# Kernel tuning notes

Measured on AMD Instinct MI355X. Metric: run time of the kernel, lower is better.

The kernel has to match this reference:

```python
import jax, jax.numpy as jnp
import numpy as np
import math

L, D, H, DK, DFF, B, S = 4, 512, 8, 256, 2048, 8, 256
HD = H * DK
EPS = 1e-6


def _norm(x, alpha, bias):
    # torch: alpha*(x-mean)/(std_unbiased + eps) + bias  (std uses ddof=1)
    mu = x.mean(axis=-1, keepdims=True)
    var = ((x - mu) ** 2).sum(axis=-1, keepdims=True) / (x.shape[-1] - 1)
    return alpha * (x - mu) / (jnp.sqrt(var) + EPS) + bias


def _positional_encoding():
    pos = jnp.arange(S, dtype=jnp.float32)[:, None]          # [S,1]
    i = jnp.arange(0, D, 2, dtype=jnp.float32)               # even indices
    pe_sin = jnp.sin(pos / (S ** (2.0 * i / D)))             # [S,D/2]
    pe_cos = jnp.cos(pos / (S ** (2.0 * (i + 1.0) / D)))     # [S,D/2]
    pe = jnp.zeros((S, D), dtype=jnp.float32)
    pe = pe.at[:, 0::2].set(pe_sin).at[:, 1::2].set(pe_cos)
    return pe


def setup_inputs() -> dict:
    key = jax.random.key(0)
    ks = jax.random.split(key, 16)
    sc = 0.02
    inp = {
        "data": jax.random.normal(ks[0], (B, S, D), dtype=jnp.float32),
        "attn_m": jax.random.randint(ks[1], (B, S), 0, 2, dtype=jnp.int32),
        "view_idx": 0,
        "seg_emb": jax.random.normal(ks[2], (3, D), dtype=jnp.float32) * sc,
        "Wq": jax.random.normal(ks[3], (L, D, HD), dtype=jnp.float32) * sc,
        "bq": jnp.zeros((L, HD), dtype=jnp.float32),
        "Wk": jax.random.normal(ks[4], (L, D, HD), dtype=jnp.float32) * sc,
        "bk": jnp.zeros((L, HD), dtype=jnp.float32),
        "Wv": jax.random.normal(ks[5], (L, D, HD), dtype=jnp.float32) * sc,
        "bv": jnp.zeros((L, HD), dtype=jnp.float32),
        "Wo": jax.random.normal(ks[6], (L, HD, D), dtype=jnp.float32) * sc,
        "bo": jnp.zeros((L, D), dtype=jnp.float32),
        "W1": jax.random.normal(ks[7], (L, D, DFF), dtype=jnp.float32) * sc,
        "b1": jnp.zeros((L, DFF), dtype=jnp.float32),
        "W2": jax.random.normal(ks[8], (L, DFF, D), dtype=jnp.float32) * sc,
        "b2": jnp.zeros((L, D), dtype=jnp.float32),
        "alpha1": jnp.ones((L, D), dtype=jnp.float32),
        "bias1": jnp.zeros((L, D), dtype=jnp.float32),
        "alpha2": jnp.ones((L, D), dtype=jnp.float32),
        "bias2": jnp.zeros((L, D), dtype=jnp.float32),
        "alpha_f": jnp.ones((D,), dtype=jnp.float32),
        "bias_f": jnp.zeros((D,), dtype=jnp.float32),
    }
    return inp


def reference(data, attn_m, view_idx, seg_emb, Wq, bq, Wk, bk, Wv, bv, Wo, bo,
              W1, b1, W2, b2, alpha1, bias1, alpha2, bias2, alpha_f, bias_f):
    # positional encoder: x*sqrt(d_f) + pe + seg_embedding(view_idx*seq_len)
    pe = _positional_encoding()
    seg_idx = view_idx * S  # scalar; must be < 3 (view_idx == 0 in practice)
    x = data * math.sqrt(D) + pe[None, :, :] + seg_emb[seg_idx][None, None, :]

    # mask: attn_m [B,S] -> [B,1,1,S] bool, True = masked (key axis)
    maskb = attn_m.astype(bool)[:, None, None, :]

    for i in range(L):
        x2 = _norm(x, alpha1[i], bias1[i])
        q = (x2 @ Wq[i] + bq[i]).reshape(B, S, H, DK).transpose(0, 2, 1, 3)
        k = (x2 @ Wk[i] + bk[i]).reshape(B, S, H, DK).transpose(0, 2, 1, 3)
        v = (x2 @ Wv[i] + bv[i]).reshape(B, S, H, DK).transpose(0, 2, 1, 3)
        scores = jnp.einsum('bhqd,bhkd->bhqk', q, k) / math.sqrt(DK)
        scores = jnp.where(maskb, -1e9, scores)
        attnw = jax.nn.softmax(scores, axis=-1)
        o = jnp.einsum('bhqk,bhkd->bhqd', attnw, v)
        o = o.transpose(0, 2, 1, 3).reshape(B, S, HD) @ Wo[i] + bo[i]
        x = x + o
        x2 = _norm(x, alpha2[i], bias2[i])
        ff = jax.nn.relu(x2 @ W1[i] + b1[i]) @ W2[i] + b2[i]
        x = x + ff

    return _norm(x, alpha_f, bias_f)
```

## Files before the change

### kernel.cpp

```cpp
#include <hip/hip_runtime.h>
#include <hip/hip_bf16.h>

#define LNUM 4
#define DIM  512
#define SS   256

typedef unsigned short ushort_t;
typedef __attribute__((ext_vector_type(8))) short bf16x8;
typedef __attribute__((ext_vector_type(4))) float f32x4;

#define VWAIT(n) asm volatile("s_waitcnt vmcnt(" #n ")" ::: "memory")
__device__ __forceinline__ void bar() { __builtin_amdgcn_s_barrier(); }

__device__ __forceinline__ ushort_t f2b(float f) {
  union { float f; unsigned u; } x; x.f = f;
  unsigned r = x.u + 0x7FFFu + ((x.u >> 16) & 1u);
  return (ushort_t)(r >> 16);
}

__device__ __forceinline__ void gload16(const void* g, void* s) {
  __builtin_amdgcn_global_load_lds((const __attribute__((address_space(1))) void*)g,
                                   (__attribute__((address_space(3))) void*)s, 16, 0, 0);
}

template<int TM, int TN, int EPI>
__global__ __launch_bounds__(256, 2)
void gemm_bt(const ushort_t* __restrict__ A, const ushort_t* __restrict__ B,
             const float* __restrict__ bias, const float* __restrict__ bias2,
             const float* __restrict__ bias3,
             ushort_t* __restrict__ outB, ushort_t* __restrict__ outB2,
             ushort_t* __restrict__ outB3, float* __restrict__ outF,
             int K, int lda, int ldb, int ldc, int nkz, int relu)
{
  constexpr int CA = TM / 32, CB = TN / 32, SN = CA + CB;
  constexpr int WM = TM / 32, WN = TN / 32;
  __shared__ ushort_t As[3 * TM * 64];
  __shared__ ushort_t Bs[3 * TN * 64];
  const int tid = threadIdx.x, lane = tid & 63, wid = tid >> 6;
  const int wm = wid >> 1, wn = wid & 1;
  const int kz = blockIdx.z, Kz = K / nkz, k0 = kz * Kz, nt = Kz >> 6;

  const ushort_t* Ab = A + (long)blockIdx.y * TM * lda + k0;
  const ushort_t* Bb = B + (long)blockIdx.x * TN * ldb + k0;

  const ushort_t* srcA[CA]; ushort_t* ldsA[CA];
  const ushort_t* srcB[CB]; ushort_t* ldsB[CB];
#pragma unroll
  for (int c = 0; c < CA; ++c) {
    int off = c * 4096 + tid * 16;
    int row = off >> 7;
    int scol = ((off & 127) ^ ((row & 7) << 4)) >> 1;
    srcA[c] = Ab + (long)row * lda + scol;
    ldsA[c] = As + c * 2048 + wid * 512;
  }
#pragma unroll
  for (int c = 0; c < CB; ++c) {
    int off = c * 4096 + tid * 16;
    int row = off >> 7;
    int scol = ((off & 127) ^ ((row & 7) << 4)) >> 1;
    srcB[c] = Bb + (long)row * ldb + scol;
    ldsB[c] = Bs + c * 2048 + wid * 512;
  }

  f32x4 acc[WM][WN] = {};

  auto STAGE = [&](int buf, int t) {
#pragma unroll
    for (int c = 0; c < CA; ++c) gload16(srcA[c] + t * 64, ldsA[c] + buf * TM * 64);
#pragma unroll
    for (int c = 0; c < CB; ++c) gload16(srcB[c] + t * 64, ldsB[c] + buf * TN * 64);
  };

  STAGE(0, 0);
  STAGE(1, 1);
  for (int t = 0; t < nt; ++t) {
    if (t < nt - 1) { if constexpr (SN == 6) VWAIT(6); else VWAIT(4); }
    else VWAIT(0);
    bar();
    if (t + 2 < nt) STAGE((t + 2) % 3, t + 2);
    const int buf = t % 3;
#pragma unroll
    for (int ks = 0; ks < 2; ++ks) {
      const int kb = ks * 64 + ((lane >> 4) << 4);
      bf16x8 af[WM], bfr[WN];
#pragma unroll
      for (int f = 0; f < WM; ++f) {
        int ra = wm * (TM / 2) + f * 16 + (lane & 15);
        af[f] = *(const bf16x8*)((const char*)As + buf * TM * 128 + ra * 128 + (kb ^ ((ra & 7) << 4)));
      }
#pragma unroll
      for (int g = 0; g < WN; ++g) {
        int rb = wn * (TN / 2) + g * 16 + (lane & 15);
        bfr[g] = *(const bf16x8*)((const char*)Bs + buf * TN * 128 + rb * 128 + (kb ^ ((rb & 7) << 4)));
      }
#pragma unroll
      for (int i = 0; i < WM; ++i)
#pragma unroll
        for (int j = 0; j < WN; ++j)
          acc[i][j] = __builtin_amdgcn_mfma_f32_16x16x32_bf16(af[i], bfr[j], acc[i][j], 0, 0, 0);
    }
  }

  const int row0 = blockIdx.y * TM + wm * (TM / 2) + ((lane >> 4) << 2);
  int col0 = blockIdx.x * TN + wn * (TN / 2) + (lane & 15);
  const float* bsel = bias;
  ushort_t* osel = outB;
  int seg = 0;
  if (EPI == 3) {
    seg = (blockIdx.x * TN) >> 11;
    if (seg == 1) { bsel = bias2; osel = outB2; }
    else if (seg == 2) { bsel = bias3; }
    col0 -= seg * 2048;
  }
#pragma unroll
  for (int i = 0; i < WM; ++i) {
#pragma unroll
    for (int j = 0; j < WN; ++j) {
      const int col = col0 + j * 16;
      float bv;
      if (EPI == 2) bv = (kz == 0) ? bias[col] : 0.f;
      else          bv = bsel[col];
#pragma unroll
      for (int r = 0; r < 4; ++r) {
        const int row = row0 + i * 16 + r;
        float v = acc[i][j][r] + bv;
        if (EPI == 2) {
          outF[(long)kz * 1048576 + (long)row * ldc + col] = v;
        } else if (EPI == 3 && seg == 2) {
          int bh = ((row >> 8) << 3) + (col >> 8);
          outB3[((long)bh << 16) + (long)(col & 255) * 256 + (row & 255)] = f2b(v);
        } else {
          if (relu) v = fmaxf(v, 0.f);
          osel[(long)row * ldc + col] = f2b(v);
        }
      }
    }
  }
}

__global__ __launch_bounds__(256)
void attn_k(const ushort_t* __restrict__ qb, const ushort_t* __restrict__ kbf,
            const ushort_t* __restrict__ vT, const int* __restrict__ attnm,
            ushort_t* __restrict__ ao)
{
  __shared__ ushort_t Qs[64 * 256];
  __shared__ ushort_t KV[3][64 * 256];
  __shared__ int smask[256];
  const int qt = blockIdx.x, bh = blockIdx.y, b = bh >> 3, h = bh & 7;
  const int tid = threadIdx.x, lane = tid & 63, wid = tid >> 6;

  smask[tid] = attnm[b * 256 + tid];
  VWAIT(0);

  int srow[8], scol[8];
#pragma unroll
  for (int c = 0; c < 8; ++c) {
    int off = c * 4096 + tid * 16;
    srow[c] = off >> 9;
    scol[c] = ((off & 511) ^ ((srow[c] & 7) << 4)) >> 1;
  }

#define STQ() do { _Pragma("unroll") for (int c = 0; c < 8; ++c) \
  gload16(qb + (long)(b * 256 + qt * 64 + srow[c]) * 2048 + h * 256 + scol[c], Qs + c * 2048 + wid * 512); } while (0)
#define STK(KC, DST) do { _Pragma("unroll") for (int c = 0; c < 8; ++c) \
  gload16(kbf + (long)(b * 256 + (KC) * 64 + srow[c]) * 2048 + h * 256 + scol[c], (DST) + c * 2048 + wid * 512); } while (0)
#define STV(VC, DST) do { _Pragma("unroll") for (int c = 0; c < 8; ++c) \
  gload16(vT + ((long)bh << 16) + (long)((VC) * 64 + srow[c]) * 256 + scol[c], (DST) + c * 2048 + wid * 512); } while (0)

  f32x4 accs[16] = {};
  f32x4 acco[4][4] = {};

#define QKC(IDX, KVB) do { _Pragma("unroll") \
  for (int ks = 0; ks < 8; ++ks) { \
    const int kb = ks * 64 + ((lane >> 4) << 4); \
    const int ra = wid * 16 + (lane & 15); \
    bf16x8 aq = *(const bf16x8*)((const char*)Qs + ra * 512 + (kb ^ ((ra & 7) << 4))); \
    _Pragma("unroll") \
    for (int j = 0; j < 4; ++j) { \
      const int rb = j * 16 + (lane & 15); \
      bf16x8 bk_ = *(const bf16x8*)((const char*)(KVB) + rb * 512 + (kb ^ ((rb & 7) << 4))); \
      accs[(IDX) * 4 + j] = __builtin_amdgcn_mfma_f32_16x16x32_bf16(aq, bk_, accs[(IDX) * 4 + j], 0, 0, 0); \
    } \
  } } while (0)

#define PVC(VC, KVB) do { _Pragma("unroll") \
  for (int ks = 0; ks < 8; ++ks) { \
    const int kb = ks * 64 + ((lane >> 4) << 4); \
    const int ra = wid * 16 + (lane & 15); \
    bf16x8 pa = *(const bf16x8*)((const char*)Qs + ra * 512 + (kb ^ ((ra & 7) << 4))); \
    _Pragma("unroll") \
    for (int j = 0; j < 4; ++j) { \
      const int rb = j * 16 + (lane & 15); \
      bf16x8 bv_ = *(const bf16x8*)((const char*)(KVB) + rb * 512 + (kb ^ ((rb & 7) << 4))); \
      acco[VC][j] = __builtin_amdgcn_mfma_f32_16x16x32_bf16(pa, bv_, acco[VC][j], 0, 0, 0); \
    } \
  } } while (0)

  STQ(); STK(0, KV[0]); STK(1, KV[1]);

  VWAIT(16); bar(); STK(2, KV[2]); QKC(0, KV[0]);
  VWAIT(8);  bar(); STK(3, KV[0]); QKC(1, KV[1]);
  VWAIT(8);  bar(); STV(0, KV[1]); QKC(2, KV[2]);
  VWAIT(8);  bar(); STV(1, KV[2]); QKC(3, KV[0]);

  bar();
  STV(2, KV[0]);

  {
    float mr[4] = {-3e38f, -3e38f, -3e38f, -3e38f}, sr[4] = {};
#pragma unroll
    for (int jj = 0; jj < 16; ++jj) {
      int key = jj * 16 + (lane & 15);
      bool mk = smask[key] != 0;
#pragma unroll
      for (int r = 0; r < 4; ++r) {
        float s = mk ? -1e9f : accs[jj][r] * 0.0625f;
        accs[jj][r] = s;
        mr[r] = fmaxf(mr[r], s);
      }
    }
#pragma unroll
    for (int o = 1; o < 16; o <<= 1)
#pragma unroll
      for (int r = 0; r < 4; ++r) mr[r] = fmaxf(mr[r], __shfl_xor(mr[r], o, 64));
#pragma unroll
    for (int jj = 0; jj < 16; ++jj)
#pragma unroll
      for (int r = 0; r < 4; ++r) {
        float e = __expf(accs[jj][r] - mr[r]);
        accs[jj][r] = e;
        sr[r] += e;
      }
#pragma unroll
    for (int o = 1; o < 16; o <<= 1)
#pragma unroll
      for (int r = 0; r < 4; ++r) sr[r] += __shfl_xor(sr[r], o, 64);
#pragma unroll
    for (int r = 0; r < 4; ++r) sr[r] = 1.f / sr[r];
#pragma unroll
    for (int jj = 0; jj < 16; ++jj)
#pragma unroll
      for (int r = 0; r < 4; ++r) {
        int prow = wid * 16 + ((lane >> 4) << 2) + r;
        int cb = (jj * 16 + (lane & 15)) * 2;
        *(ushort_t*)((char*)Qs + prow * 512 + (cb ^ ((prow & 7) << 4))) = f2b(accs[jj][r] * sr[r]);
      }
  }

  VWAIT(16); bar();                 PVC(0, KV[1]);
  VWAIT(8);  bar(); STV(3, KV[1]); PVC(1, KV[2]);
  VWAIT(8);  bar();                 PVC(2, KV[0]);
  VWAIT(0);  bar();                 PVC(3, KV[1]);

#pragma unroll
  for (int vc = 0; vc < 4; ++vc)
#pragma unroll
    for (int j = 0; j < 4; ++j)
#pragma unroll
      for (int r = 0; r < 4; ++r) {
        int q = qt * 64 + wid * 16 + ((lane >> 4) << 2) + r;
        int dk = vc * 64 + j * 16 + (lane & 15);
        ao[(long)(b * 256 + q) * 2048 + h * 256 + dk] = f2b(acco[vc][j][r]);
      }
#undef STQ
#undef STK
#undef STV
#undef QKC
#undef PVC
}

__global__ __launch_bounds__(256)
void build_x(const float* __restrict__ data, const float* __restrict__ seg,
             const int* __restrict__ viewp, float* __restrict__ x)
{
  int i = blockIdx.x * 256 + threadIdx.x;
  int d = i & 511;
  int s = (i >> 9) & 255;
  float ang = (float)s * exp2f((float)d * -0.03125f);
  float pe = (d & 1) ? cosf(ang) : sinf(ang);
  int vrow = viewp[0] * SS;
  x[i] = data[i] * 22.627416997969522f + pe + seg[vrow * DIM + d];
}

__global__ __launch_bounds__(256)
void lnorm_k(const float* __restrict__ x, const float* __restrict__ p0,
             const float* __restrict__ p1, float* __restrict__ xout,
             const float* __restrict__ alpha, const float* __restrict__ beta,
             ushort_t* __restrict__ outB, float* __restrict__ outF)
{
  const int row = blockIdx.x, tid = threadIdx.x;
  const long base = (long)row * DIM;
  float2 v = ((const float2*)(x + base))[tid];
  if (p0) {
    float2 a = ((const float2*)(p0 + base))[tid];
    float2 c = ((const float2*)(p1 + base))[tid];
    v.x += a.x + c.x; v.y += a.y + c.y;
    ((float2*)(xout + base))[tid] = v;
  }
  float s = v.x + v.y;
#pragma unroll
  for (int o = 32; o; o >>= 1) s += __shfl_xor(s, o, 64);
  __shared__ float rs[4], rq[4];
  if ((tid & 63) == 0) rs[tid >> 6] = s;
  __syncthreads();
  const float mu = (rs[0] + rs[1] + rs[2] + rs[3]) * (1.f / 512.f);
  const float dx = v.x - mu, dy = v.y - mu;
  float q = dx * dx + dy * dy;
#pragma unroll
  for (int o = 32; o; o >>= 1) q += __shfl_xor(q, o, 64);
  if ((tid & 63) == 0) rq[tid >> 6] = q;
  __syncthreads();
  const float var = (rq[0] + rq[1] + rq[2] + rq[3]) * (1.f / 511.f);
  const float rstd = 1.f / (sqrtf(var) + 1e-6f);
  const int d0 = tid * 2;
  const float o0 = alpha[d0] * dx * rstd + beta[d0];
  const float o1 = alpha[d0 + 1] * dy * rstd + beta[d0 + 1];
  if (outB) { outB[base + d0] = f2b(o0); outB[base + d0 + 1] = f2b(o1); }
  else      { outF[base + d0] = o0;      outF[base + d0 + 1] = o1; }
}

__global__ __launch_bounds__(256)
void wtrans(const float* __restrict__ in, ushort_t* __restrict__ out,
            int R, int C, long ozs)
{
  __shared__ float t[32][33];
  const int z = blockIdx.z;
  const long zi = (long)z * R * C, zo = (long)z * ozs;
  const int c0 = blockIdx.x * 32, r0 = blockIdx.y * 32;
  const int tx = threadIdx.x & 31, ty = threadIdx.x >> 5;
#pragma unroll
  for (int i = 0; i < 4; ++i) t[ty + i * 8][tx] = in[zi + (long)(r0 + ty + i * 8) * C + c0 + tx];
  __syncthreads();
#pragma unroll
  for (int i = 0; i < 4; ++i) out[zo + (long)(c0 + ty + i * 8) * R + r0 + tx] = f2b(t[tx][ty + i * 8]);
}

extern "C" void kernel_launch(void* const* d_in, const int* in_sizes, int n_in,
                              void* d_out, int out_size, void* d_ws, size_t ws_size,
                              hipStream_t stream)
{
  const float* data  = (const float*)d_in[0];
  const int*   attnm = (const int*)d_in[1];
  const int*   viewp = (const int*)d_in[2];
  const float* seg   = (const float*)d_in[3];
  const float* Wq    = (const float*)d_in[4];
  const float* bq    = (const float*)d_in[5];
  const float* Wk    = (const float*)d_in[6];
  const float* bk    = (const float*)d_in[7];
  const float* Wv    = (const float*)d_in[8];
  const float* bv    = (const float*)d_in[9];
  const float* Wo    = (const float*)d_in[10];
  const float* bo    = (const float*)d_in[11];
  const float* W1    = (const float*)d_in[12];
  const float* b1    = (const float*)d_in[13];
  const float* W2    = (const float*)d_in[14];
  const float* b2    = (const float*)d_in[15];
  const float* al1   = (const float*)d_in[16];
  const float* be1   = (const float*)d_in[17];
  const float* al2   = (const float*)d_in[18];
  const float* be2   = (const float*)d_in[19];
  const float* alf   = (const float*)d_in[20];
  const float* bef   = (const float*)d_in[21];

  char* w = (char*)d_ws;
  const size_t MB = 1024 * 1024;
  ushort_t* qkvW = (ushort_t*)(w + 0 * MB);
  ushort_t* WoT  = (ushort_t*)(w + 24 * MB);
  ushort_t* W1T  = (ushort_t*)(w + 32 * MB);
  ushort_t* W2T  = (ushort_t*)(w + 40 * MB);
  float*    x    = (float*)   (w + 48 * MB);
  ushort_t* x2   = (ushort_t*)(w + 52 * MB);
  ushort_t* qb   = (ushort_t*)(w + 54 * MB);
  ushort_t* kbf  = (ushort_t*)(w + 62 * MB);
  ushort_t* vT   = (ushort_t*)(w + 70 * MB);
  ushort_t* ao   = (ushort_t*)(w + 78 * MB);
  ushort_t* ffh  = (ushort_t*)(w + 86 * MB);
  float*    pA   = (float*)   (w + 94 * MB);
  float*    pB   = (float*)   (w + 98 * MB);

  dim3 blk(256);
  const long QKV_L = 6144L * 512;
  wtrans<<<dim3(64, 16, 4), blk, 0, stream>>>(Wq, qkvW + 0 * 2048 * 512, 512, 2048, QKV_L);
  wtrans<<<dim3(64, 16, 4), blk, 0, stream>>>(Wk, qkvW + 1 * 2048 * 512, 512, 2048, QKV_L);
  wtrans<<<dim3(64, 16, 4), blk, 0, stream>>>(Wv, qkvW + 2 * 2048 * 512, 512, 2048, QKV_L);
  wtrans<<<dim3(16, 64, 4), blk, 0, stream>>>(Wo, WoT, 2048, 512, 512L * 2048);
  wtrans<<<dim3(64, 16, 4), blk, 0, stream>>>(W1, W1T, 512, 2048, 2048L * 512);
  wtrans<<<dim3(16, 64, 4), blk, 0, stream>>>(W2, W2T, 2048, 512, 512L * 2048);
  build_x<<<4096, blk, 0, stream>>>(data, seg, viewp, x);

  for (int i = 0; i < LNUM; ++i) {
    if (i == 0)
      lnorm_k<<<2048, blk, 0, stream>>>(x, nullptr, nullptr, nullptr,
                                        al1, be1, x2, nullptr);
    gemm_bt<128, 64, 3><<<dim3(96, 16, 1), blk, 0, stream>>>(
        x2, qkvW + (long)i * QKV_L, bq + i * 2048, bk + i * 2048, bv + i * 2048,
        qb, kbf, vT, nullptr, 512, 512, 512, 2048, 1, 0);
    attn_k<<<dim3(4, 64), blk, 0, stream>>>(qb, kbf, vT, attnm, ao);
    gemm_bt<64, 64, 2><<<dim3(8, 32, 2), blk, 0, stream>>>(
        ao, WoT + (long)i * 512 * 2048, bo + i * 512, nullptr, nullptr,
        nullptr, nullptr, nullptr, pA, 2048, 2048, 2048, 512, 2, 0);
    lnorm_k<<<2048, blk, 0, stream>>>(x, pA, pB, x, al2 + i * 512, be2 + i * 512, x2, nullptr);
    gemm_bt<128, 64, 0><<<dim3(32, 16, 1), blk, 0, stream>>>(
        x2, W1T + (long)i * 2048 * 512, b1 + i * 2048, nullptr, nullptr,
        ffh, nullptr, nullptr, nullptr, 512, 512, 512, 2048, 1, 1);
    gemm_bt<64, 64, 2><<<dim3(8, 32, 2), blk, 0, stream>>>(
        ffh, W2T + (long)i * 512 * 2048, b2 + i * 512, nullptr, nullptr,
        nullptr, nullptr, nullptr, pA, 2048, 2048, 2048, 512, 2, 0);
    if (i < LNUM - 1)
      lnorm_k<<<2048, blk, 0, stream>>>(x, pA, pB, x, al1 + (i + 1) * 512, be1 + (i + 1) * 512, x2, nullptr);
    else
      lnorm_k<<<2048, blk, 0, stream>>>(x, pA, pB, x, alf, bef, nullptr, (float*)d_out);
  }
}
```

Before: 474.6 us.

## Stage V transpose through LDS, raise MFMA priority, split-K four ways

The QKV GEMM epilogue for the V segment now writes the biased bf16 tile transposed into shared memory and then stores contiguous 16-byte chunks to the transposed V buffer. This replaces scattered 2-byte strided global writes. s_setprio is raised around the MFMA blocks in both the GEMM and attention kernels so matrix work gets issue priority over other waves. The Wo and W2 GEMMs move from split-K 2 to 4 to launch more blocks, and layernorm sums a variable number of fp32 partials, which costs extra partial-buffer traffic.

```diff
diff --git a/kernel.cpp b/kernel.cpp
--- a/kernel.cpp
+++ b/kernel.cpp
@@ -8,6 +8,7 @@
 typedef unsigned short ushort_t;
 typedef __attribute__((ext_vector_type(8))) short bf16x8;
 typedef __attribute__((ext_vector_type(4))) float f32x4;
+typedef __attribute__((ext_vector_type(8))) unsigned short u16x8;
 
 #define VWAIT(n) asm volatile("s_waitcnt vmcnt(" #n ")" ::: "memory")
 __device__ __forceinline__ void bar() { __builtin_amdgcn_s_barrier(); }
@@ -93,11 +94,13 @@
         int rb = wn * (TN / 2) + g * 16 + (lane & 15);
         bfr[g] = *(const bf16x8*)((const char*)Bs + buf * TN * 128 + rb * 128 + (kb ^ ((rb & 7) << 4)));
       }
+      __builtin_amdgcn_s_setprio(1);
 #pragma unroll
       for (int i = 0; i < WM; ++i)
 #pragma unroll
         for (int j = 0; j < WN; ++j)
           acc[i][j] = __builtin_amdgcn_mfma_f32_16x16x32_bf16(af[i], bfr[j], acc[i][j], 0, 0, 0);
+      __builtin_amdgcn_s_setprio(0);
     }
   }
 
@@ -112,6 +115,36 @@
     else if (seg == 2) { bsel = bias3; }
     col0 -= seg * 2048;
   }
+
+  if (EPI == 3 && seg == 2) {
+    ushort_t* Vt = As;
+    bar();
+#pragma unroll
+    for (int i = 0; i < WM; ++i)
+#pragma unroll
+      for (int j = 0; j < WN; ++j) {
+        const int colL = wn * (TN / 2) + j * 16 + (lane & 15);
+        const float bv = bsel[(col0 + j * 16) & 2047];
+#pragma unroll
+        for (int r = 0; r < 4; ++r) {
+          const int rowL = wm * (TM / 2) + i * 16 + ((lane >> 4) << 2) + r;
+          Vt[colL * 136 + rowL] = f2b(acc[i][j][r] + bv);
+        }
+      }
+    bar();
+    const int colvBase = blockIdx.x * TN - 4096;
+    const int h = colvBase >> 8, dk0 = colvBase & 255;
+    const int rowBase = blockIdx.y * TM;
+    const int bh = ((rowBase >> 8) << 3) + h;
+    const int s0 = rowBase & 255;
+    const int dkl = tid >> 2, scc = (tid & 3) * 32;
+    ushort_t* dst = outB3 + ((long)bh << 16) + (long)(dk0 + dkl) * 256 + s0 + scc;
+#pragma unroll
+    for (int m = 0; m < 4; ++m)
+      *(u16x8*)(dst + m * 8) = *(const u16x8*)(Vt + dkl * 136 + scc + m * 8);
+    return;
+  }
+
 #pragma unroll
   for (int i = 0; i < WM; ++i) {
 #pragma unroll
@@ -126,9 +159,6 @@
         float v = acc[i][j][r] + bv;
         if (EPI == 2) {
           outF[(long)kz * 1048576 + (long)row * ldc + col] = v;
-        } else if (EPI == 3 && seg == 2) {
-          int bh = ((row >> 8) << 3) + (col >> 8);
-          outB3[((long)bh << 16) + (long)(col & 255) * 256 + (row & 255)] = f2b(v);
         } else {
           if (relu) v = fmaxf(v, 0.f);
           osel[(long)row * ldc + col] = f2b(v);
@@ -170,7 +200,7 @@
   f32x4 accs[16] = {};
   f32x4 acco[4][4] = {};
 
-#define QKC(IDX, KVB) do { _Pragma("unroll") \
+#define QKC(IDX, KVB) do { __builtin_amdgcn_s_setprio(1); _Pragma("unroll") \
   for (int ks = 0; ks < 8; ++ks) { \
     const int kb = ks * 64 + ((lane >> 4) << 4); \
     const int ra = wid * 16 + (lane & 15); \
@@ -181,9 +211,9 @@
       bf16x8 bk_ = *(const bf16x8*)((const char*)(KVB) + rb * 512 + (kb ^ ((rb & 7) << 4))); \
       accs[(IDX) * 4 + j] = __builtin_amdgcn_mfma_f32_16x16x32_bf16(aq, bk_, accs[(IDX) * 4 + j], 0, 0, 0); \
     } \
-  } } while (0)
-
-#define PVC(VC, KVB) do { _Pragma("unroll") \
+  } __builtin_amdgcn_s_setprio(0); } while (0)
+
+#define PVC(VC, KVB) do { __builtin_amdgcn_s_setprio(1); _Pragma("unroll") \
   for (int ks = 0; ks < 8; ++ks) { \
     const int kb = ks * 64 + ((lane >> 4) << 4); \
     const int ra = wid * 16 + (lane & 15); \
@@ -194,7 +224,7 @@
       bf16x8 bv_ = *(const bf16x8*)((const char*)(KVB) + rb * 512 + (kb ^ ((rb & 7) << 4))); \
       acco[VC][j] = __builtin_amdgcn_mfma_f32_16x16x32_bf16(pa, bv_, acco[VC][j], 0, 0, 0); \
     } \
-  } } while (0)
+  } __builtin_amdgcn_s_setprio(0); } while (0)
 
   STQ(); STK(0, KV[0]); STK(1, KV[1]);
 
@@ -283,18 +313,19 @@
 }
 
 __global__ __launch_bounds__(256)
-void lnorm_k(const float* __restrict__ x, const float* __restrict__ p0,
-             const float* __restrict__ p1, float* __restrict__ xout,
+void lnorm_k(const float* __restrict__ x, const float* __restrict__ parts, int np,
+             float* __restrict__ xout,
              const float* __restrict__ alpha, const float* __restrict__ beta,
              ushort_t* __restrict__ outB, float* __restrict__ outF)
 {
   const int row = blockIdx.x, tid = threadIdx.x;
   const long base = (long)row * DIM;
   float2 v = ((const float2*)(x + base))[tid];
-  if (p0) {
-    float2 a = ((const float2*)(p0 + base))[tid];
-    float2 c = ((const float2*)(p1 + base))[tid];
-    v.x += a.x + c.x; v.y += a.y + c.y;
+  if (np) {
+    for (int p = 0; p < np; ++p) {
+      float2 a = ((const float2*)(parts + (long)p * 1048576 + base))[tid];
+      v.x += a.x; v.y += a.y;
+    }
     ((float2*)(xout + base))[tid] = v;
   }
   float s = v.x + v.y;
@@ -375,8 +406,7 @@
   ushort_t* vT   = (ushort_t*)(w + 70 * MB);
   ushort_t* ao   = (ushort_t*)(w + 78 * MB);
   ushort_t* ffh  = (ushort_t*)(w + 86 * MB);
-  float*    pA   = (float*)   (w + 94 * MB);
-  float*    pB   = (float*)   (w + 98 * MB);
+  float*    parts= (float*)   (w + 94 * MB);
 
   dim3 blk(256);
   const long QKV_L = 6144L * 512;
@@ -390,25 +420,24 @@
 
   for (int i = 0; i < LNUM; ++i) {
     if (i == 0)
-      lnorm_k<<<2048, blk, 0, stream>>>(x, nullptr, nullptr, nullptr,
-                                        al1, be1, x2, nullptr);
+      lnorm_k<<<2048, blk, 0, stream>>>(x, nullptr, 0, nullptr, al1, be1, x2, nullptr);
     gemm_bt<128, 64, 3><<<dim3(96, 16, 1), blk, 0, stream>>>(
         x2, qkvW + (long)i * QKV_L, bq + i * 2048, bk + i * 2048, bv + i * 2048,
         qb, kbf, vT, nullptr, 512, 512, 512, 2048, 1, 0);
     attn_k<<<dim3(4, 64), blk, 0, stream>>>(qb, kbf, vT, attnm, ao);
-    gemm_bt<64, 64, 2><<<dim3(8, 32, 2), blk, 0, stream>>>(
+    gemm_bt<64, 64, 2><<<dim3(8, 32, 4), blk, 0, stream>>>(
         ao, WoT + (long)i * 512 * 2048, bo + i * 512, nullptr, nullptr,
-        nullptr, nullptr, nullptr, pA, 2048, 2048, 2048, 512, 2, 0);
-    lnorm_k<<<2048, blk, 0, stream>>>(x, pA, pB, x, al2 + i * 512, be2 + i * 512, x2, nullptr);
+        nullptr, nullptr, nullptr, parts, 2048, 2048, 2048, 512, 4, 0);
+    lnorm_k<<<2048, blk, 0, stream>>>(x, parts, 4, x, al2 + i * 512, be2 + i * 512, x2, nullptr);
     gemm_bt<128, 64, 0><<<dim3(32, 16, 1), blk, 0, stream>>>(
         x2, W1T + (long)i * 2048 * 512, b1 + i * 2048, nullptr, nullptr,
         ffh, nullptr, nullptr, nullptr, 512, 512, 512, 2048, 1, 1);
-    gemm_bt<64, 64, 2><<<dim3(8, 32, 2), blk, 0, stream>>>(
+    gemm_bt<64, 64, 2><<<dim3(8, 32, 4), blk, 0, stream>>>(
         ffh, W2T + (long)i * 512 * 2048, b2 + i * 512, nullptr, nullptr,
-        nullptr, nullptr, nullptr, pA, 2048, 2048, 2048, 512, 2, 0);
+        nullptr, nullptr, nullptr, parts, 2048, 2048, 2048, 512, 4, 0);
     if (i < LNUM - 1)
-      lnorm_k<<<2048, blk, 0, stream>>>(x, pA, pB, x, al1 + (i + 1) * 512, be1 + (i + 1) * 512, x2, nullptr);
+      lnorm_k<<<2048, blk, 0, stream>>>(x, parts, 4, x, al1 + (i + 1) * 512, be1 + (i + 1) * 512, x2, nullptr);
     else
-      lnorm_k<<<2048, blk, 0, stream>>>(x, pA, pB, x, alf, bef, nullptr, (float*)d_out);
-  }
-}
+      lnorm_k<<<2048, blk, 0, stream>>>(x, parts, 4, x, alf, bef, nullptr, (float*)d_out);
+  }
+}
```

New measurement: 451.9 us. -4.8%, faster.
